# Kernel tuning notes

Hardware: AMD Instinct MI355X
Metric: run time of the kernel (lower is better)

The kernel has to match this reference:

```python
import jax, jax.numpy as jnp
import numpy as np

N = 100000      # nodes
E = 1600000     # edges (avg degree 16)
R = 4           # num_relations
NB = 30         # num_bases
F_IN = 86       # num_node_features
H = 128         # hidden_dim
C = 18          # N_CLASSES
G = 512         # graphs in batch


def setup_inputs() -> dict:
    key = jax.random.key(0)
    ks = jax.random.split(key, 14)
    x = jax.random.normal(ks[0], (N, F_IN), dtype=jnp.float32)
    edge_index = jax.random.randint(ks[1], (2, E), 0, N, dtype=jnp.int32)
    edge_type = jax.random.randint(ks[2], (E,), 0, R, dtype=jnp.int32)
    batch = jnp.sort(jax.random.randint(ks[3], (N,), 0, G, dtype=jnp.int32))
    s_in = 1.0 / np.sqrt(F_IN)
    s_h = 1.0 / np.sqrt(H)
    s_b = 1.0 / np.sqrt(NB)
    basis1 = jax.random.normal(ks[4], (NB, F_IN, H), jnp.float32) * s_in
    comp1 = jax.random.normal(ks[5], (R, NB), jnp.float32) * s_b
    root1 = jax.random.normal(ks[6], (F_IN, H), jnp.float32) * s_in
    bias1 = jnp.zeros((H,), jnp.float32)
    basis2 = jax.random.normal(ks[7], (NB, H, H), jnp.float32) * s_h
    comp2 = jax.random.normal(ks[8], (R, NB), jnp.float32) * s_b
    root2 = jax.random.normal(ks[9], (H, H), jnp.float32) * s_h
    bias2 = jnp.zeros((H,), jnp.float32)
    fc_w = jax.random.normal(ks[10], (H, C), jnp.float32) * s_h
    fc_b = jnp.zeros((C,), jnp.float32)
    return {"x": x, "edge_index": edge_index, "edge_type": edge_type, "batch": batch,
            "basis1": basis1, "comp1": comp1, "root1": root1, "bias1": bias1,
            "basis2": basis2, "comp2": comp2, "root2": root2, "bias2": bias2,
            "fc_w": fc_w, "fc_b": fc_b}


def rgcn_conv(x, edge_index, edge_type, basis, comp, root, bias):
    # PyG RGCNConv with basis decomposition, aggr='mean' (per-relation mean, summed over relations)
    n = x.shape[0]
    W = jnp.einsum('rb,bio->rio', comp, basis)          # [R, in, out]
    xw = jnp.einsum('ni,rio->rno', x, W)                # [R, N, out] relation-specific transforms
    src, dst = edge_index[0], edge_index[1]
    msg = xw[edge_type, src]                            # [E, out] gather per edge
    seg = edge_type.astype(jnp.int32) * n + dst          # segment per (relation, dst-node)
    sums = jax.ops.segment_sum(msg, seg, num_segments=R * n)          # [R*N, out]
    cnt = jax.ops.segment_sum(jnp.ones((msg.shape[0],), msg.dtype), seg, num_segments=R * n)
    mean = sums / jnp.maximum(cnt, 1.0)[:, None]
    agg = mean.reshape(R, n, -1).sum(axis=0)            # sum over relations
    return agg + x @ root + bias


def reference(x, edge_index, edge_type, batch, basis1, comp1, root1, bias1,
              basis2, comp2, root2, bias2, fc_w, fc_b):
    h = jax.nn.relu(rgcn_conv(x, edge_index, edge_type, basis1, comp1, root1, bias1))
    h = rgcn_conv(h, edge_index, edge_type, basis2, comp2, root2, bias2)
    g = jax.ops.segment_sum(h, batch, num_segments=G)   # global_add_pool -> [G, H]
    g = jax.nn.relu(g @ fc_w + fc_b)
    # dropout is identity in eval mode
    return jax.nn.log_softmax(g, axis=1)
```

## Files before the change

### kernel.cpp

```cpp
#include <hip/hip_runtime.h>
#include <hip/hip_bf16.h>
#include <cstddef>
#include <cstdint>

#define N_NODES 100000
#define N_ROWS  100032
#define DUMMY   100000
#define N_EDGES 1600000
#define N_REL   4
#define N_BASES 30
#define FIN     86
#define HID     128
#define N_CLS   18
#define N_GRAPH 512
#define KCAT    640
#define BM      32
#define NKK     (KCAT / 32)

#define SEG (N_REL * N_NODES)
#define SSRC_MAX (N_EDGES + 3 * SEG)
#define SCAN_CHUNK 1024
#define NB_SCAN ((SEG + SCAN_CHUNK - 1) / SCAN_CHUNK)

typedef __attribute__((ext_vector_type(8))) short bf16x8;
typedef __attribute__((ext_vector_type(4))) float f32x4;

__device__ inline float blo(unsigned int u) {
    union { unsigned int i; float f; } c; c.i = u << 16; return c.f;
}
__device__ inline float bhi(unsigned int u) {
    union { unsigned int i; float f; } c; c.i = u & 0xffff0000u; return c.f;
}
__device__ inline unsigned short f2bf(float f) {
    __hip_bfloat16 h = __float2bfloat16(f);
    return *reinterpret_cast<unsigned short*>(&h);
}
__device__ inline unsigned int pk2(float lo, float hi) {
    return (unsigned int)f2bf(lo) | ((unsigned int)f2bf(hi) << 16);
}
__device__ inline int pad4i(int x) { return (x + 3) & ~3; }

template <int KV>
__global__ void k_wt(const float* __restrict__ basis, const float* __restrict__ comp,
                     const float* __restrict__ root, short* __restrict__ Wt) {
    int id = blockIdx.x * 256 + threadIdx.x;
    if (id >= KCAT * HID) return;
    int n = id & 127, s = id >> 7;
    int k = s & 127, blk = s >> 7;
    float v = 0.f;
    if (k < KV) {
        if (blk < N_REL) {
#pragma unroll
            for (int b = 0; b < N_BASES; ++b)
                v += comp[blk * N_BASES + b] * basis[((size_t)b * KV + k) * HID + n];
        } else {
            v = root[k * HID + n];
        }
    }
    Wt[(size_t)n * KCAT + s] = (short)f2bf(v);
}

__global__ void k_xcvt(const float* __restrict__ x, short* __restrict__ X0,
                       short* __restrict__ H1) {
    int id = blockIdx.x * 256 + threadIdx.x;
    if (id >= N_ROWS * HID) return;
    int n = id >> 7, k = id & 127;
    float v = (n < N_NODES && k < FIN) ? x[n * FIN + k] : 0.f;
    X0[id] = (short)f2bf(v);
    if (n >= N_NODES) H1[id] = 0;
}

__global__ void k_fill(int* __restrict__ p) {
    int i = blockIdx.x * 256 + threadIdx.x;
    if (i < SSRC_MAX) p[i] = DUMMY;
}

__global__ void k_count(const int* __restrict__ et, const int* __restrict__ dst,
                        int* __restrict__ cnt, int* __restrict__ rank) {
    int e = blockIdx.x * 256 + threadIdx.x;
    if (e >= N_EDGES) return;
    rank[e] = atomicAdd(cnt + et[e] * N_NODES + dst[e], 1);
}

__global__ void k_bsum(const int* __restrict__ cnt, int* __restrict__ bsum) {
    __shared__ int red[256];
    int base = blockIdx.x * SCAN_CHUNK + threadIdx.x * 4;
    int s = 0;
#pragma unroll
    for (int j = 0; j < 4; j++) { int idx = base + j; if (idx < SEG) s += pad4i(cnt[idx]); }
    red[threadIdx.x] = s;
    __syncthreads();
    for (int w = 128; w > 0; w >>= 1) {
        if (threadIdx.x < w) red[threadIdx.x] += red[threadIdx.x + w];
        __syncthreads();
    }
    if (threadIdx.x == 0) bsum[blockIdx.x] = red[0];
}

__global__ void k_bpref(int* __restrict__ bsum, int nb) {
    __shared__ int s[512];
    int t = threadIdx.x;
    int v = (t < nb) ? bsum[t] : 0;
    s[t] = v;
    __syncthreads();
    for (int d = 1; d < 512; d <<= 1) {
        int add = (t >= d) ? s[t - d] : 0;
        __syncthreads();
        s[t] += add;
        __syncthreads();
    }
    if (t < nb) bsum[t] = s[t] - v;
}

__global__ void k_offsets(const int* __restrict__ cnt, const int* __restrict__ bpref,
                          int* __restrict__ off) {
    __shared__ int tp[256];
    int t = threadIdx.x;
    int base = blockIdx.x * SCAN_CHUNK + t * 4;
    int v[4], s = 0;
#pragma unroll
    for (int j = 0; j < 4; j++) { int idx = base + j; v[j] = (idx < SEG) ? pad4i(cnt[idx]) : 0; s += v[j]; }
    tp[t] = s;
    __syncthreads();
    if (t == 0) { int run = 0; for (int i = 0; i < 256; i++) { int x = tp[i]; tp[i] = run; run += x; } }
    __syncthreads();
    int p = bpref[blockIdx.x] + tp[t];
#pragma unroll
    for (int j = 0; j < 4; j++) { int idx = base + j; if (idx < SEG) off[idx] = p; p += v[j]; }
}

__global__ void k_scatter(const int* __restrict__ et, const int* __restrict__ srcI,
                          const int* __restrict__ dstI, const int* __restrict__ off,
                          const int* __restrict__ rank, int* __restrict__ ssrc) {
    int e = blockIdx.x * 256 + threadIdx.x;
    if (e >= N_EDGES) return;
    int seg = et[e] * N_NODES + dstI[e];
    ssrc[off[seg] + rank[e]] = srcI[e];
}

template <int MODE>
__launch_bounds__(512, 4)
__global__ void k_fused(const short* __restrict__ F,
                        const int* __restrict__ off, const int* __restrict__ cnt,
                        const int* __restrict__ ssrc,
                        const short* __restrict__ Wt,
                        const float* __restrict__ bias,
                        short* __restrict__ H,
                        const int* __restrict__ batch, float* __restrict__ g) {
    __shared__ short As[BM * KCAT];
    char* Ab = reinterpret_cast<char*>(As);
    const int tid = threadIdx.x;
    const int m0 = blockIdx.x * BM;

    {
        const int row = tid >> 4, cu = tid & 15;
        uint4 v = *reinterpret_cast<const uint4*>(F + (size_t)(m0 + row) * HID + cu * 8);
        const int p = (row * 1280 + 1024 + cu * 16) ^ ((row & 7) << 4);
        *reinterpret_cast<uint4*>(Ab + p) = v;
    }

    {
        const int G = tid >> 4, q = tid & 15;
        const int node = m0 + G;
        if (node < N_NODES) {
            const int pbase = G * 1280 + q * 16;
            const int swz = (G & 7) << 4;
            for (int r = 0; r < N_REL; ++r) {
                const int seg = r * N_NODES + node;
                const int o0 = off[seg], c = cnt[seg];
                float a[8];
#pragma unroll
                for (int j = 0; j < 8; ++j) a[j] = 0.f;
                const int4* sp = reinterpret_cast<const int4*>(ssrc + o0);
                const int nch = (c + 3) >> 2;
                for (int ch = 0; ch < nch; ++ch) {
                    int4 e4 = sp[ch];
                    uint4 v0 = *reinterpret_cast<const uint4*>(F + (size_t)e4.x * HID + q * 8);
                    uint4 v1 = *reinterpret_cast<const uint4*>(F + (size_t)e4.y * HID + q * 8);
                    uint4 v2 = *reinterpret_cast<const uint4*>(F + (size_t)e4.z * HID + q * 8);
                    uint4 v3 = *reinterpret_cast<const uint4*>(F + (size_t)e4.w * HID + q * 8);
                    a[0] += blo(v0.x) + blo(v1.x) + blo(v2.x) + blo(v3.x);
                    a[1] += bhi(v0.x) + bhi(v1.x) + bhi(v2.x) + bhi(v3.x);
                    a[2] += blo(v0.y) + blo(v1.y) + blo(v2.y) + blo(v3.y);
                    a[3] += bhi(v0.y) + bhi(v1.y) + bhi(v2.y) + bhi(v3.y);
                    a[4] += blo(v0.z) + blo(v1.z) + blo(v2.z) + blo(v3.z);
                    a[5] += bhi(v0.z) + bhi(v1.z) + bhi(v2.z) + bhi(v3.z);
                    a[6] += blo(v0.w) + blo(v1.w) + blo(v2.w) + blo(v3.w);
                    a[7] += bhi(v0.w) + bhi(v1.w) + bhi(v2.w) + bhi(v3.w);
                }
                const float inv = (c > 0) ? 1.f / (float)c : 0.f;
                uint4 w;
                w.x = pk2(a[0] * inv, a[1] * inv);
                w.y = pk2(a[2] * inv, a[3] * inv);
                w.z = pk2(a[4] * inv, a[5] * inv);
                w.w = pk2(a[6] * inv, a[7] * inv);
                *reinterpret_cast<uint4*>(Ab + ((pbase + r * 256) ^ swz)) = w;
            }
        }
    }
    __syncthreads();

    const int wave = tid >> 6, lane = tid & 63;
    const int q = lane & 15, hi = lane >> 4;
    const int col = wave * 16 + q;

    bf16x8 bfrag[NKK];
    {
        const short* bp = Wt + (size_t)col * KCAT + hi * 8;
#pragma unroll
        for (int kk = 0; kk < NKK; ++kk)
            bfrag[kk] = *reinterpret_cast<const bf16x8*>(bp + kk * 32);
    }

    f32x4 acc[2];
    acc[0] = (f32x4){0.f, 0.f, 0.f, 0.f};
    acc[1] = (f32x4){0.f, 0.f, 0.f, 0.f};
    const int arow = q * 1280;
    const int bx = (hi * 16) ^ ((q & 7) << 4);
#pragma unroll
    for (int kk = 0; kk < NKK; ++kk) {
        const int bo = (kk * 64) ^ bx;
#pragma unroll
        for (int rf = 0; rf < 2; ++rf) {
            bf16x8 a = *reinterpret_cast<const bf16x8*>(Ab + arow + rf * (16 * 1280) + bo);
            acc[rf] = __builtin_amdgcn_mfma_f32_16x16x32_bf16(a, bfrag[kk], acc[rf], 0, 0, 0);
        }
    }

    if (MODE == 1) {
        const float bc = bias[col];
#pragma unroll
        for (int rf = 0; rf < 2; ++rf) {
#pragma unroll
            for (int r = 0; r < 4; ++r) {
                const int row = m0 + rf * 16 + hi * 4 + r;
                if (row < N_NODES) {
                    float v = fmaxf(acc[rf][r] + bc, 0.f);
                    H[(size_t)row * HID + col] = (short)f2bf(v);
                }
            }
        }
    } else {
        int curb = -1;
        float run = 0.f;
#pragma unroll
        for (int rf = 0; rf < 2; ++rf) {
#pragma unroll
            for (int r = 0; r < 4; ++r) {
                const int row = m0 + rf * 16 + hi * 4 + r;
                if (row < N_NODES) {
                    int b = batch[row];
                    if (b != curb) {
                        if (curb >= 0) atomicAdd(&g[curb * HID + col], run);
                        curb = b; run = 0.f;
                    }
                    run += acc[rf][r];
                }
            }
        }
        if (curb >= 0) atomicAdd(&g[curb * HID + col], run);
    }
}

__global__ void k_fc(const float* __restrict__ g, const float* __restrict__ bias2,
                     const int* __restrict__ batch, const float* __restrict__ fcw,
                     const float* __restrict__ fcb, float* __restrict__ out) {
    __shared__ float pooled[HID];
    __shared__ float vals[N_CLS];
    __shared__ float s_lse;
    __shared__ int s_cnt;
    int gi = blockIdx.x, t = threadIdx.x;
    if (t == 0) {
        int lo = 0, hi = N_NODES;
        while (lo < hi) { int m = (lo + hi) >> 1; if (batch[m] < gi) lo = m + 1; else hi = m; }
        int lo2 = lo, hi2 = N_NODES;
        while (lo2 < hi2) { int m = (lo2 + hi2) >> 1; if (batch[m] < gi + 1) lo2 = m + 1; else hi2 = m; }
        s_cnt = lo2 - lo;
    }
    __syncthreads();
    pooled[t] = g[gi * HID + t] + (float)s_cnt * bias2[t];
    __syncthreads();
    if (t < N_CLS) {
        float acc = fcb[t];
        for (int k = 0; k < HID; k++) acc = fmaf(pooled[k], fcw[k * N_CLS + t], acc);
        vals[t] = fmaxf(acc, 0.f);
    }
    __syncthreads();
    if (t == 0) {
        float m = vals[0];
        for (int c = 1; c < N_CLS; c++) m = fmaxf(m, vals[c]);
        float ssum = 0.f;
        for (int c = 0; c < N_CLS; c++) ssum += expf(vals[c] - m);
        s_lse = m + logf(ssum);
    }
    __syncthreads();
    if (t < N_CLS) out[gi * N_CLS + t] = vals[t] - s_lse;
}

extern "C" void kernel_launch(void* const* d_in, const int* in_sizes, int n_in,
                              void* d_out, int out_size, void* d_ws, size_t ws_size,
                              hipStream_t stream) {
    const float* x      = (const float*)d_in[0];
    const int*   ei     = (const int*)d_in[1];
    const int*   src    = ei;
    const int*   dst    = ei + N_EDGES;
    const int*   et     = (const int*)d_in[2];
    const int*   batch  = (const int*)d_in[3];
    const float* basis1 = (const float*)d_in[4];
    const float* comp1  = (const float*)d_in[5];
    const float* root1  = (const float*)d_in[6];
    const float* bias1  = (const float*)d_in[7];
    const float* basis2 = (const float*)d_in[8];
    const float* comp2  = (const float*)d_in[9];
    const float* root2  = (const float*)d_in[10];
    const float* bias2  = (const float*)d_in[11];
    const float* fcw    = (const float*)d_in[12];
    const float* fcb    = (const float*)d_in[13];
    float* out = (float*)d_out;

    short* X0   = (short*)d_ws;
    short* H1   = X0 + (size_t)N_ROWS * HID;
    short* Wt1  = H1 + (size_t)N_ROWS * HID;
    short* Wt2  = Wt1 + HID * KCAT;
    float* g    = (float*)(Wt2 + HID * KCAT);
    int*   cnt  = (int*)(g + N_GRAPH * HID);
    int*   off  = cnt + SEG;
    int*   bsum = off + SEG;
    int*   rank = bsum + 512;
    int*   ssrc = rank + N_EDGES;

    hipMemsetAsync(cnt, 0, SEG * sizeof(int), stream);
    hipMemsetAsync(g, 0, (size_t)N_GRAPH * HID * sizeof(float), stream);

    k_wt<FIN><<<(KCAT * HID + 255) / 256, 256, 0, stream>>>(basis1, comp1, root1, Wt1);
    k_wt<HID><<<(KCAT * HID + 255) / 256, 256, 0, stream>>>(basis2, comp2, root2, Wt2);
    k_xcvt<<<(N_ROWS * HID + 255) / 256, 256, 0, stream>>>(x, X0, H1);
    k_fill<<<(SSRC_MAX + 255) / 256, 256, 0, stream>>>(ssrc);

    k_count<<<(N_EDGES + 255) / 256, 256, 0, stream>>>(et, dst, cnt, rank);
    k_bsum<<<NB_SCAN, 256, 0, stream>>>(cnt, bsum);
    k_bpref<<<1, 512, 0, stream>>>(bsum, NB_SCAN);
    k_offsets<<<NB_SCAN, 256, 0, stream>>>(cnt, bsum, off);
    k_scatter<<<(N_EDGES + 255) / 256, 256, 0, stream>>>(et, src, dst, off, rank, ssrc);

    const int FUSED_GRID = N_ROWS / BM;

    k_fused<1><<<FUSED_GRID, 512, 0, stream>>>(X0, off, cnt, ssrc, Wt1, bias1, H1,
                                               nullptr, nullptr);
    k_fused<2><<<FUSED_GRID, 512, 0, stream>>>(H1, off, cnt, ssrc, Wt2, nullptr, nullptr,
                                               batch, g);

    k_fc<<<N_GRAPH, HID, 0, stream>>>(g, bias2, batch, fcw, fcb, out);
}
```

Measured before the change: 391.3 us.

## Fuse prep kernels, interleave relation segments per node, aggregate two relations concurrently

Merges the memsets, weight-combination, input conversion and ssrc fill into a single prep kernel to cut launch count. Reorders the (relation,dst) segment index to dst*4+rel, so each node's four offsets and counts are read with one int4 load and its edge lists sit next to each other. The aggregation now walks two relations at once with dummy-padded indices, giving eight independent gathers in flight per step. In exchange, padded iterations do extra dummy-row loads when relation degrees differ, and the weight loop is no longer unrolled.

```diff
diff --git a/kernel.cpp b/kernel.cpp
--- a/kernel.cpp
+++ b/kernel.cpp
@@ -19,11 +19,13 @@
 
 #define SEG (N_REL * N_NODES)
 #define SSRC_MAX (N_EDGES + 3 * SEG)
+#define SSRC_ALLOC (SSRC_MAX + 64)
 #define SCAN_CHUNK 1024
 #define NB_SCAN ((SEG + SCAN_CHUNK - 1) / SCAN_CHUNK)
 
 typedef __attribute__((ext_vector_type(8))) short bf16x8;
 typedef __attribute__((ext_vector_type(4))) float f32x4;
+typedef __attribute__((ext_vector_type(2))) float f32x2;
 
 __device__ inline float blo(unsigned int u) {
     union { unsigned int i; float f; } c; c.i = u << 16; return c.f;
@@ -31,6 +33,7 @@
 __device__ inline float bhi(unsigned int u) {
     union { unsigned int i; float f; } c; c.i = u & 0xffff0000u; return c.f;
 }
+__device__ inline f32x2 ubf2(unsigned int u) { return (f32x2){blo(u), bhi(u)}; }
 __device__ inline unsigned short f2bf(float f) {
     __hip_bfloat16 h = __float2bfloat16(f);
     return *reinterpret_cast<unsigned short*>(&h);
@@ -40,17 +43,22 @@
 }
 __device__ inline int pad4i(int x) { return (x + 3) & ~3; }
 
-template <int KV>
-__global__ void k_wt(const float* __restrict__ basis, const float* __restrict__ comp,
-                     const float* __restrict__ root, short* __restrict__ Wt) {
-    int id = blockIdx.x * 256 + threadIdx.x;
-    if (id >= KCAT * HID) return;
+#define PREP_R0 (N_ROWS * HID)
+#define PREP_R1 (KCAT * HID)
+#define PREP_R2 (KCAT * HID)
+#define PREP_R3 SSRC_ALLOC
+#define PREP_R4 SEG
+#define PREP_R5 (N_GRAPH * HID)
+#define PREP_TOTAL (PREP_R0 + PREP_R1 + PREP_R2 + PREP_R3 + PREP_R4 + PREP_R5)
+
+__device__ inline void wt_body(int id, int KV, const float* __restrict__ basis,
+                               const float* __restrict__ comp, const float* __restrict__ root,
+                               short* __restrict__ Wt) {
     int n = id & 127, s = id >> 7;
     int k = s & 127, blk = s >> 7;
     float v = 0.f;
     if (k < KV) {
         if (blk < N_REL) {
-#pragma unroll
             for (int b = 0; b < N_BASES; ++b)
                 v += comp[blk * N_BASES + b] * basis[((size_t)b * KV + k) * HID + n];
         } else {
@@ -60,26 +68,40 @@
     Wt[(size_t)n * KCAT + s] = (short)f2bf(v);
 }
 
-__global__ void k_xcvt(const float* __restrict__ x, short* __restrict__ X0,
-                       short* __restrict__ H1) {
+__global__ void k_prep(const float* __restrict__ x,
+                       const float* __restrict__ basis1, const float* __restrict__ comp1,
+                       const float* __restrict__ root1,
+                       const float* __restrict__ basis2, const float* __restrict__ comp2,
+                       const float* __restrict__ root2,
+                       short* __restrict__ X0, short* __restrict__ H1,
+                       short* __restrict__ Wt1, short* __restrict__ Wt2,
+                       int* __restrict__ ssrc, int* __restrict__ cnt,
+                       float* __restrict__ g) {
     int id = blockIdx.x * 256 + threadIdx.x;
-    if (id >= N_ROWS * HID) return;
-    int n = id >> 7, k = id & 127;
-    float v = (n < N_NODES && k < FIN) ? x[n * FIN + k] : 0.f;
-    X0[id] = (short)f2bf(v);
-    if (n >= N_NODES) H1[id] = 0;
-}
-
-__global__ void k_fill(int* __restrict__ p) {
-    int i = blockIdx.x * 256 + threadIdx.x;
-    if (i < SSRC_MAX) p[i] = DUMMY;
+    if (id < PREP_R0) {
+        int n = id >> 7, k = id & 127;
+        float v = (n < N_NODES && k < FIN) ? x[n * FIN + k] : 0.f;
+        X0[id] = (short)f2bf(v);
+        if (n >= N_NODES) H1[id] = 0;
+        return;
+    }
+    id -= PREP_R0;
+    if (id < PREP_R1) { wt_body(id, FIN, basis1, comp1, root1, Wt1); return; }
+    id -= PREP_R1;
+    if (id < PREP_R2) { wt_body(id, HID, basis2, comp2, root2, Wt2); return; }
+    id -= PREP_R2;
+    if (id < PREP_R3) { ssrc[id] = DUMMY; return; }
+    id -= PREP_R3;
+    if (id < PREP_R4) { cnt[id] = 0; return; }
+    id -= PREP_R4;
+    if (id < PREP_R5) g[id] = 0.f;
 }
 
 __global__ void k_count(const int* __restrict__ et, const int* __restrict__ dst,
                         int* __restrict__ cnt, int* __restrict__ rank) {
     int e = blockIdx.x * 256 + threadIdx.x;
     if (e >= N_EDGES) return;
-    rank[e] = atomicAdd(cnt + et[e] * N_NODES + dst[e], 1);
+    rank[e] = atomicAdd(cnt + dst[e] * 4 + et[e], 1);
 }
 
 __global__ void k_bsum(const int* __restrict__ cnt, int* __restrict__ bsum) {
@@ -134,8 +156,56 @@
                           const int* __restrict__ rank, int* __restrict__ ssrc) {
     int e = blockIdx.x * 256 + threadIdx.x;
     if (e >= N_EDGES) return;
-    int seg = et[e] * N_NODES + dstI[e];
+    int seg = dstI[e] * 4 + et[e];
     ssrc[off[seg] + rank[e]] = srcI[e];
+}
+
+#define ACCROW(A, v) { A[0] += ubf2(v.x); A[1] += ubf2(v.y); A[2] += ubf2(v.z); A[3] += ubf2(v.w); }
+
+__device__ __forceinline__ void agg_pair(const short* __restrict__ F,
+                                         const int* __restrict__ ssrc,
+                                         int oa, int ca, int ob, int cb,
+                                         char* Ab, int G, int q, int ra) {
+    f32x2 A0[4], A1[4];
+#pragma unroll
+    for (int j = 0; j < 4; ++j) { A0[j] = (f32x2){0.f, 0.f}; A1[j] = (f32x2){0.f, 0.f}; }
+    const int na = (ca + 3) >> 2, nb = (cb + 3) >> 2;
+    const int ia = oa >> 2, ib = ob >> 2;
+    const int nmax = na > nb ? na : nb;
+    const int4* sp = reinterpret_cast<const int4*>(ssrc);
+    const int cq = q * 8;
+    for (int t = 0; t < nmax; ++t) {
+        int4 ea = sp[ia + (t < na ? t : 0)];
+        int4 eb = sp[ib + (t < nb ? t : 0)];
+        ea.x = t < na ? ea.x : DUMMY; ea.y = t < na ? ea.y : DUMMY;
+        ea.z = t < na ? ea.z : DUMMY; ea.w = t < na ? ea.w : DUMMY;
+        eb.x = t < nb ? eb.x : DUMMY; eb.y = t < nb ? eb.y : DUMMY;
+        eb.z = t < nb ? eb.z : DUMMY; eb.w = t < nb ? eb.w : DUMMY;
+        const uint4 va0 = *reinterpret_cast<const uint4*>(F + (size_t)ea.x * HID + cq);
+        const uint4 va1 = *reinterpret_cast<const uint4*>(F + (size_t)ea.y * HID + cq);
+        const uint4 va2 = *reinterpret_cast<const uint4*>(F + (size_t)ea.z * HID + cq);
+        const uint4 va3 = *reinterpret_cast<const uint4*>(F + (size_t)ea.w * HID + cq);
+        const uint4 vb0 = *reinterpret_cast<const uint4*>(F + (size_t)eb.x * HID + cq);
+        const uint4 vb1 = *reinterpret_cast<const uint4*>(F + (size_t)eb.y * HID + cq);
+        const uint4 vb2 = *reinterpret_cast<const uint4*>(F + (size_t)eb.z * HID + cq);
+        const uint4 vb3 = *reinterpret_cast<const uint4*>(F + (size_t)eb.w * HID + cq);
+        ACCROW(A0, va0); ACCROW(A0, va1); ACCROW(A0, va2); ACCROW(A0, va3);
+        ACCROW(A1, vb0); ACCROW(A1, vb1); ACCROW(A1, vb2); ACCROW(A1, vb3);
+    }
+    const float inva = (ca > 0) ? 1.f / (float)ca : 0.f;
+    const float invb = (cb > 0) ? 1.f / (float)cb : 0.f;
+    uint4 wa, wb;
+    wa.x = pk2(A0[0].x * inva, A0[0].y * inva);
+    wa.y = pk2(A0[1].x * inva, A0[1].y * inva);
+    wa.z = pk2(A0[2].x * inva, A0[2].y * inva);
+    wa.w = pk2(A0[3].x * inva, A0[3].y * inva);
+    wb.x = pk2(A1[0].x * invb, A1[0].y * invb);
+    wb.y = pk2(A1[1].x * invb, A1[1].y * invb);
+    wb.z = pk2(A1[2].x * invb, A1[2].y * invb);
+    wb.w = pk2(A1[3].x * invb, A1[3].y * invb);
+    const int swz = (G & 7) << 4;
+    *reinterpret_cast<uint4*>(Ab + (G * 1280 + ((ra * 256 + q * 16) ^ swz))) = wa;
+    *reinterpret_cast<uint4*>(Ab + (G * 1280 + (((ra + 1) * 256 + q * 16) ^ swz))) = wb;
 }
 
 template <int MODE>
@@ -163,39 +233,10 @@
         const int G = tid >> 4, q = tid & 15;
         const int node = m0 + G;
         if (node < N_NODES) {
-            const int pbase = G * 1280 + q * 16;
-            const int swz = (G & 7) << 4;
-            for (int r = 0; r < N_REL; ++r) {
-                const int seg = r * N_NODES + node;
-                const int o0 = off[seg], c = cnt[seg];
-                float a[8];
-#pragma unroll
-                for (int j = 0; j < 8; ++j) a[j] = 0.f;
-                const int4* sp = reinterpret_cast<const int4*>(ssrc + o0);
-                const int nch = (c + 3) >> 2;
-                for (int ch = 0; ch < nch; ++ch) {
-                    int4 e4 = sp[ch];
-                    uint4 v0 = *reinterpret_cast<const uint4*>(F + (size_t)e4.x * HID + q * 8);
-                    uint4 v1 = *reinterpret_cast<const uint4*>(F + (size_t)e4.y * HID + q * 8);
-                    uint4 v2 = *reinterpret_cast<const uint4*>(F + (size_t)e4.z * HID + q * 8);
-                    uint4 v3 = *reinterpret_cast<const uint4*>(F + (size_t)e4.w * HID + q * 8);
-                    a[0] += blo(v0.x) + blo(v1.x) + blo(v2.x) + blo(v3.x);
-                    a[1] += bhi(v0.x) + bhi(v1.x) + bhi(v2.x) + bhi(v3.x);
-                    a[2] += blo(v0.y) + blo(v1.y) + blo(v2.y) + blo(v3.y);
-                    a[3] += bhi(v0.y) + bhi(v1.y) + bhi(v2.y) + bhi(v3.y);
-                    a[4] += blo(v0.z) + blo(v1.z) + blo(v2.z) + blo(v3.z);
-                    a[5] += bhi(v0.z) + bhi(v1.z) + bhi(v2.z) + bhi(v3.z);
-                    a[6] += blo(v0.w) + blo(v1.w) + blo(v2.w) + blo(v3.w);
-                    a[7] += bhi(v0.w) + bhi(v1.w) + bhi(v2.w) + bhi(v3.w);
-                }
-                const float inv = (c > 0) ? 1.f / (float)c : 0.f;
-                uint4 w;
-                w.x = pk2(a[0] * inv, a[1] * inv);
-                w.y = pk2(a[2] * inv, a[3] * inv);
-                w.z = pk2(a[4] * inv, a[5] * inv);
-                w.w = pk2(a[6] * inv, a[7] * inv);
-                *reinterpret_cast<uint4*>(Ab + ((pbase + r * 256) ^ swz)) = w;
-            }
+            const int4 o4 = *reinterpret_cast<const int4*>(off + node * 4);
+            const int4 c4 = *reinterpret_cast<const int4*>(cnt + node * 4);
+            agg_pair(F, ssrc, o4.x, c4.x, o4.y, c4.y, Ab, G, q, 0);
+            agg_pair(F, ssrc, o4.z, c4.z, o4.w, c4.w, Ab, G, q, 2);
         }
     }
     __syncthreads();
@@ -329,13 +370,9 @@
     int*   rank = bsum + 512;
     int*   ssrc = rank + N_EDGES;
 
-    hipMemsetAsync(cnt, 0, SEG * sizeof(int), stream);
-    hipMemsetAsync(g, 0, (size_t)N_GRAPH * HID * sizeof(float), stream);
-
-    k_wt<FIN><<<(KCAT * HID + 255) / 256, 256, 0, stream>>>(basis1, comp1, root1, Wt1);
-    k_wt<HID><<<(KCAT * HID + 255) / 256, 256, 0, stream>>>(basis2, comp2, root2, Wt2);
-    k_xcvt<<<(N_ROWS * HID + 255) / 256, 256, 0, stream>>>(x, X0, H1);
-    k_fill<<<(SSRC_MAX + 255) / 256, 256, 0, stream>>>(ssrc);
+    k_prep<<<(PREP_TOTAL + 255) / 256, 256, 0, stream>>>(
+        x, basis1, comp1, root1, basis2, comp2, root2,
+        X0, H1, Wt1, Wt2, ssrc, cnt, g);
 
     k_count<<<(N_EDGES + 255) / 256, 256, 0, stream>>>(et, dst, cnt, rank);
     k_bsum<<<NB_SCAN, 256, 0, stream>>>(cnt, bsum);
```

Result: no change. 395.1 us (+1.0%).

## Build CSR via per-tile counting sort and merge prep kernels

Applied to the files above, without the earlier changes.

Replaces the global per-(relation,node) counting-sort CSR build, which needed atomics on a 400K-entry counter array, a multi-kernel scan and a full DUMMY fill, with a two-level scheme. Edges are first bucketed per 32-node tile with atomics on a small tile counter array and a single-block scan. Each tile is then sorted locally in shared memory by (node, relation), and the sort writes node-major off/cnt arrays plus its own padding. Weight building, feature conversion and zeroing are merged into one prep kernel. The fused kernels now load four offsets per node as an int4 and prefetch the first index chunks. The cost is an extra intermediate edge buffer pass, and the local sort serialises a 128-bucket prefix on one thread.

```diff
diff --git a/kernel.cpp b/kernel.cpp
--- a/kernel.cpp
+++ b/kernel.cpp
@@ -17,10 +17,11 @@
 #define BM      32
 #define NKK     (KCAT / 32)
 
-#define SEG (N_REL * N_NODES)
-#define SSRC_MAX (N_EDGES + 3 * SEG)
-#define SCAN_CHUNK 1024
-#define NB_SCAN ((SEG + SCAN_CHUNK - 1) / SCAN_CHUNK)
+#define NTILE   (N_ROWS / BM)
+#define NTILEP  3200
+#define TPAD    (3 * 128)
+#define SEGP    (NTILE * 128)
+#define SSRC_ALLOC (N_EDGES + NTILE * (TPAD + 4) + 64)
 
 typedef __attribute__((ext_vector_type(8))) short bf16x8;
 typedef __attribute__((ext_vector_type(4))) float f32x4;
@@ -38,19 +39,22 @@
 __device__ inline unsigned int pk2(float lo, float hi) {
     return (unsigned int)f2bf(lo) | ((unsigned int)f2bf(hi) << 16);
 }
-__device__ inline int pad4i(int x) { return (x + 3) & ~3; }
-
-template <int KV>
-__global__ void k_wt(const float* __restrict__ basis, const float* __restrict__ comp,
-                     const float* __restrict__ root, short* __restrict__ Wt) {
-    int id = blockIdx.x * 256 + threadIdx.x;
-    if (id >= KCAT * HID) return;
+
+#define PREP_R0 (N_ROWS * HID)
+#define PREP_R1 (KCAT * HID)
+#define PREP_R2 (KCAT * HID)
+#define PREP_R3 NTILEP
+#define PREP_R4 (N_GRAPH * HID)
+#define PREP_TOTAL (PREP_R0 + PREP_R1 + PREP_R2 + PREP_R3 + PREP_R4)
+
+__device__ inline void wt_body(int id, int KV, const float* __restrict__ basis,
+                               const float* __restrict__ comp, const float* __restrict__ root,
+                               short* __restrict__ Wt) {
     int n = id & 127, s = id >> 7;
     int k = s & 127, blk = s >> 7;
     float v = 0.f;
     if (k < KV) {
         if (blk < N_REL) {
-#pragma unroll
             for (int b = 0; b < N_BASES; ++b)
                 v += comp[blk * N_BASES + b] * basis[((size_t)b * KV + k) * HID + n];
         } else {
@@ -60,82 +64,149 @@
     Wt[(size_t)n * KCAT + s] = (short)f2bf(v);
 }
 
-__global__ void k_xcvt(const float* __restrict__ x, short* __restrict__ X0,
-                       short* __restrict__ H1) {
+__global__ void k_prep(const float* __restrict__ x,
+                       const float* __restrict__ basis1, const float* __restrict__ comp1,
+                       const float* __restrict__ root1,
+                       const float* __restrict__ basis2, const float* __restrict__ comp2,
+                       const float* __restrict__ root2,
+                       short* __restrict__ X0, short* __restrict__ H1,
+                       short* __restrict__ Wt1, short* __restrict__ Wt2,
+                       int* __restrict__ tilecnt, float* __restrict__ g) {
     int id = blockIdx.x * 256 + threadIdx.x;
-    if (id >= N_ROWS * HID) return;
-    int n = id >> 7, k = id & 127;
-    float v = (n < N_NODES && k < FIN) ? x[n * FIN + k] : 0.f;
-    X0[id] = (short)f2bf(v);
-    if (n >= N_NODES) H1[id] = 0;
-}
-
-__global__ void k_fill(int* __restrict__ p) {
-    int i = blockIdx.x * 256 + threadIdx.x;
-    if (i < SSRC_MAX) p[i] = DUMMY;
-}
-
-__global__ void k_count(const int* __restrict__ et, const int* __restrict__ dst,
-                        int* __restrict__ cnt, int* __restrict__ rank) {
+    if (id < PREP_R0) {
+        int n = id >> 7, k = id & 127;
+        float v = (n < N_NODES && k < FIN) ? x[n * FIN + k] : 0.f;
+        X0[id] = (short)f2bf(v);
+        if (n >= N_NODES) H1[id] = 0;
+        return;
+    }
+    id -= PREP_R0;
+    if (id < PREP_R1) { wt_body(id, FIN, basis1, comp1, root1, Wt1); return; }
+    id -= PREP_R1;
+    if (id < PREP_R2) { wt_body(id, HID, basis2, comp2, root2, Wt2); return; }
+    id -= PREP_R2;
+    if (id < PREP_R3) { tilecnt[id] = 0; return; }
+    id -= PREP_R3;
+    if (id < PREP_R4) g[id] = 0.f;
+}
+
+__global__ void k_tilecnt(const int* __restrict__ dst, int* __restrict__ tilecnt,
+                          int* __restrict__ rank) {
     int e = blockIdx.x * 256 + threadIdx.x;
     if (e >= N_EDGES) return;
-    rank[e] = atomicAdd(cnt + et[e] * N_NODES + dst[e], 1);
-}
-
-__global__ void k_bsum(const int* __restrict__ cnt, int* __restrict__ bsum) {
-    __shared__ int red[256];
-    int base = blockIdx.x * SCAN_CHUNK + threadIdx.x * 4;
-    int s = 0;
-#pragma unroll
-    for (int j = 0; j < 4; j++) { int idx = base + j; if (idx < SEG) s += pad4i(cnt[idx]); }
-    red[threadIdx.x] = s;
-    __syncthreads();
-    for (int w = 128; w > 0; w >>= 1) {
-        if (threadIdx.x < w) red[threadIdx.x] += red[threadIdx.x + w];
+    rank[e] = atomicAdd(tilecnt + (dst[e] >> 5), 1);
+}
+
+__global__ void k_tilescan(const int* __restrict__ tilecnt, int* __restrict__ rawoff,
+                           int* __restrict__ obase) {
+    __shared__ int s1[1024], s2[1024];
+    int t = threadIdx.x;
+    int base = t * 4;
+    int v[4], w[4], sum1 = 0, sum2 = 0;
+#pragma unroll
+    for (int j = 0; j < 4; ++j) {
+        v[j] = (base + j < NTILE) ? tilecnt[base + j] : 0;
+        w[j] = ((v[j] + 3) & ~3) + TPAD;
+        sum1 += v[j]; sum2 += w[j];
+    }
+    s1[t] = sum1; s2[t] = sum2;
+    __syncthreads();
+    for (int d = 1; d < 1024; d <<= 1) {
+        int a1 = (t >= d) ? s1[t - d] : 0;
+        int a2 = (t >= d) ? s2[t - d] : 0;
         __syncthreads();
-    }
-    if (threadIdx.x == 0) bsum[blockIdx.x] = red[0];
-}
-
-__global__ void k_bpref(int* __restrict__ bsum, int nb) {
-    __shared__ int s[512];
-    int t = threadIdx.x;
-    int v = (t < nb) ? bsum[t] : 0;
-    s[t] = v;
-    __syncthreads();
-    for (int d = 1; d < 512; d <<= 1) {
-        int add = (t >= d) ? s[t - d] : 0;
+        s1[t] += a1; s2[t] += a2;
         __syncthreads();
-        s[t] += add;
-        __syncthreads();
-    }
-    if (t < nb) bsum[t] = s[t] - v;
-}
-
-__global__ void k_offsets(const int* __restrict__ cnt, const int* __restrict__ bpref,
-                          int* __restrict__ off) {
-    __shared__ int tp[256];
-    int t = threadIdx.x;
-    int base = blockIdx.x * SCAN_CHUNK + t * 4;
-    int v[4], s = 0;
-#pragma unroll
-    for (int j = 0; j < 4; j++) { int idx = base + j; v[j] = (idx < SEG) ? pad4i(cnt[idx]) : 0; s += v[j]; }
-    tp[t] = s;
-    __syncthreads();
-    if (t == 0) { int run = 0; for (int i = 0; i < 256; i++) { int x = tp[i]; tp[i] = run; run += x; } }
-    __syncthreads();
-    int p = bpref[blockIdx.x] + tp[t];
-#pragma unroll
-    for (int j = 0; j < 4; j++) { int idx = base + j; if (idx < SEG) off[idx] = p; p += v[j]; }
-}
-
-__global__ void k_scatter(const int* __restrict__ et, const int* __restrict__ srcI,
-                          const int* __restrict__ dstI, const int* __restrict__ off,
-                          const int* __restrict__ rank, int* __restrict__ ssrc) {
+    }
+    int p1 = s1[t] - sum1, p2 = s2[t] - sum2;
+#pragma unroll
+    for (int j = 0; j < 4; ++j) {
+        if (base + j < NTILE) {
+            rawoff[base + j] = p1;
+            obase[base + j] = p2;
+            p1 += v[j]; p2 += w[j];
+        }
+    }
+}
+
+__global__ void k_tilescatter(const int* __restrict__ et, const int* __restrict__ srcI,
+                              const int* __restrict__ dstI, const int* __restrict__ rank,
+                              const int* __restrict__ rawoff, int2* __restrict__ ebuf) {
     int e = blockIdx.x * 256 + threadIdx.x;
     if (e >= N_EDGES) return;
-    int seg = et[e] * N_NODES + dstI[e];
-    ssrc[off[seg] + rank[e]] = srcI[e];
+    int d = dstI[e];
+    int t = d >> 5;
+    int key = ((d & 31) << 2) | et[e];
+    int2 rec; rec.x = srcI[e]; rec.y = key;
+    ebuf[rawoff[t] + rank[e]] = rec;
+}
+
+__global__ void k_tilesort(const int2* __restrict__ ebuf, const int* __restrict__ tilecnt,
+                           const int* __restrict__ rawoff, const int* __restrict__ obase,
+                           int* __restrict__ ssrc, int* __restrict__ off,
+                           int* __restrict__ cnt) {
+    __shared__ int hist[128], boff[128], cur[128];
+    const int t = blockIdx.x, tid = threadIdx.x;
+    const int n = tilecnt[t];
+    const int base_in = rawoff[t];
+    const int base_out = obase[t];
+    if (tid < 128) { hist[tid] = 0; cur[tid] = 0; }
+    __syncthreads();
+    for (int i = tid; i < n; i += 256)
+        atomicAdd(&hist[ebuf[base_in + i].y], 1);
+    __syncthreads();
+    if (tid == 0) {
+        int run = 0;
+        for (int b = 0; b < 128; ++b) { boff[b] = run; run += (hist[b] + 3) & ~3; }
+    }
+    __syncthreads();
+    for (int i = tid; i < n; i += 256) {
+        int2 e = ebuf[base_in + i];
+        int p = atomicAdd(&cur[e.y], 1);
+        ssrc[base_out + boff[e.y] + p] = e.x;
+    }
+    if (tid < 128) {
+        int b = tid, h = hist[b], bo = base_out + boff[b];
+        int hp = (h + 3) & ~3;
+        for (int j = h; j < hp; ++j) ssrc[bo + j] = DUMMY;
+        off[t * 128 + b] = bo;
+        cnt[t * 128 + b] = h;
+    }
+}
+
+__device__ __forceinline__ void agg_one(const short* __restrict__ F,
+                                        const int4* __restrict__ sp,
+                                        int o, int c, int4 e4,
+                                        char* Ab, int G, int q, int r) {
+    float a[8];
+#pragma unroll
+    for (int j = 0; j < 8; ++j) a[j] = 0.f;
+    const int cq = q * 8;
+    const int nch = (c + 3) >> 2;
+    const int ib = o >> 2;
+    for (int ch = 0; ch < nch; ++ch) {
+        if (ch) e4 = sp[ib + ch];
+        uint4 v0 = *reinterpret_cast<const uint4*>(F + (size_t)e4.x * HID + cq);
+        uint4 v1 = *reinterpret_cast<const uint4*>(F + (size_t)e4.y * HID + cq);
+        uint4 v2 = *reinterpret_cast<const uint4*>(F + (size_t)e4.z * HID + cq);
+        uint4 v3 = *reinterpret_cast<const uint4*>(F + (size_t)e4.w * HID + cq);
+        a[0] += blo(v0.x); a[1] += bhi(v0.x); a[2] += blo(v0.y); a[3] += bhi(v0.y);
+        a[4] += blo(v0.z); a[5] += bhi(v0.z); a[6] += blo(v0.w); a[7] += bhi(v0.w);
+        a[0] += blo(v1.x); a[1] += bhi(v1.x); a[2] += blo(v1.y); a[3] += bhi(v1.y);
+        a[4] += blo(v1.z); a[5] += bhi(v1.z); a[6] += blo(v1.w); a[7] += bhi(v1.w);
+        a[0] += blo(v2.x); a[1] += bhi(v2.x); a[2] += blo(v2.y); a[3] += bhi(v2.y);
+        a[4] += blo(v2.z); a[5] += bhi(v2.z); a[6] += blo(v2.w); a[7] += bhi(v2.w);
+        a[0] += blo(v3.x); a[1] += bhi(v3.x); a[2] += blo(v3.y); a[3] += bhi(v3.y);
+        a[4] += blo(v3.z); a[5] += bhi(v3.z); a[6] += blo(v3.w); a[7] += bhi(v3.w);
+    }
+    const float inv = (c > 0) ? 1.f / (float)c : 0.f;
+    uint4 w;
+    w.x = pk2(a[0] * inv, a[1] * inv);
+    w.y = pk2(a[2] * inv, a[3] * inv);
+    w.z = pk2(a[4] * inv, a[5] * inv);
+    w.w = pk2(a[6] * inv, a[7] * inv);
+    const int swz = (G & 7) << 4;
+    *reinterpret_cast<uint4*>(Ab + (G * 1280 + ((r * 256 + q * 16) ^ swz))) = w;
 }
 
 template <int MODE>
@@ -151,58 +222,35 @@
     char* Ab = reinterpret_cast<char*>(As);
     const int tid = threadIdx.x;
     const int m0 = blockIdx.x * BM;
+    const int G = tid >> 4, q = tid & 15;
+    const int node = m0 + G;
+
+    int4 o4 = (int4){0, 0, 0, 0}, c4 = (int4){0, 0, 0, 0};
+    const int4* sp = reinterpret_cast<const int4*>(ssrc);
+    if (node < N_NODES) {
+        o4 = *reinterpret_cast<const int4*>(off + node * 4);
+        c4 = *reinterpret_cast<const int4*>(cnt + node * 4);
+    }
+    int4 pre0 = sp[o4.x >> 2];
+    int4 pre1 = sp[o4.y >> 2];
 
     {
-        const int row = tid >> 4, cu = tid & 15;
-        uint4 v = *reinterpret_cast<const uint4*>(F + (size_t)(m0 + row) * HID + cu * 8);
-        const int p = (row * 1280 + 1024 + cu * 16) ^ ((row & 7) << 4);
+        uint4 v = *reinterpret_cast<const uint4*>(F + (size_t)(m0 + G) * HID + q * 8);
+        const int p = (G * 1280 + 1024 + q * 16) ^ ((G & 7) << 4);
         *reinterpret_cast<uint4*>(Ab + p) = v;
     }
 
-    {
-        const int G = tid >> 4, q = tid & 15;
-        const int node = m0 + G;
-        if (node < N_NODES) {
-            const int pbase = G * 1280 + q * 16;
-            const int swz = (G & 7) << 4;
-            for (int r = 0; r < N_REL; ++r) {
-                const int seg = r * N_NODES + node;
-                const int o0 = off[seg], c = cnt[seg];
-                float a[8];
-#pragma unroll
-                for (int j = 0; j < 8; ++j) a[j] = 0.f;
-                const int4* sp = reinterpret_cast<const int4*>(ssrc + o0);
-                const int nch = (c + 3) >> 2;
-                for (int ch = 0; ch < nch; ++ch) {
-                    int4 e4 = sp[ch];
-                    uint4 v0 = *reinterpret_cast<const uint4*>(F + (size_t)e4.x * HID + q * 8);
-                    uint4 v1 = *reinterpret_cast<const uint4*>(F + (size_t)e4.y * HID + q * 8);
-                    uint4 v2 = *reinterpret_cast<const uint4*>(F + (size_t)e4.z * HID + q * 8);
-                    uint4 v3 = *reinterpret_cast<const uint4*>(F + (size_t)e4.w * HID + q * 8);
-                    a[0] += blo(v0.x) + blo(v1.x) + blo(v2.x) + blo(v3.x);
-                    a[1] += bhi(v0.x) + bhi(v1.x) + bhi(v2.x) + bhi(v3.x);
-                    a[2] += blo(v0.y) + blo(v1.y) + blo(v2.y) + blo(v3.y);
-                    a[3] += bhi(v0.y) + bhi(v1.y) + bhi(v2.y) + bhi(v3.y);
-                    a[4] += blo(v0.z) + blo(v1.z) + blo(v2.z) + blo(v3.z);
-                    a[5] += bhi(v0.z) + bhi(v1.z) + bhi(v2.z) + bhi(v3.z);
-                    a[6] += blo(v0.w) + blo(v1.w) + blo(v2.w) + blo(v3.w);
-                    a[7] += bhi(v0.w) + bhi(v1.w) + bhi(v2.w) + bhi(v3.w);
-                }
-                const float inv = (c > 0) ? 1.f / (float)c : 0.f;
-                uint4 w;
-                w.x = pk2(a[0] * inv, a[1] * inv);
-                w.y = pk2(a[2] * inv, a[3] * inv);
-                w.z = pk2(a[4] * inv, a[5] * inv);
-                w.w = pk2(a[6] * inv, a[7] * inv);
-                *reinterpret_cast<uint4*>(Ab + ((pbase + r * 256) ^ swz)) = w;
-            }
-        }
+    if (node < N_NODES) {
+        agg_one(F, sp, o4.x, c4.x, pre0, Ab, G, q, 0);
+        agg_one(F, sp, o4.y, c4.y, pre1, Ab, G, q, 1);
+        agg_one(F, sp, o4.z, c4.z, sp[o4.z >> 2], Ab, G, q, 2);
+        agg_one(F, sp, o4.w, c4.w, sp[o4.w >> 2], Ab, G, q, 3);
     }
     __syncthreads();
 
     const int wave = tid >> 6, lane = tid & 63;
-    const int q = lane & 15, hi = lane >> 4;
-    const int col = wave * 16 + q;
+    const int ql = lane & 15, hi = lane >> 4;
+    const int col = wave * 16 + ql;
 
     bf16x8 bfrag[NKK];
     {
@@ -215,8 +263,8 @@
     f32x4 acc[2];
     acc[0] = (f32x4){0.f, 0.f, 0.f, 0.f};
     acc[1] = (f32x4){0.f, 0.f, 0.f, 0.f};
-    const int arow = q * 1280;
-    const int bx = (hi * 16) ^ ((q & 7) << 4);
+    const int arow = ql * 1280;
+    const int bx = (hi * 16) ^ ((ql & 7) << 4);
 #pragma unroll
     for (int kk = 0; kk < NKK; ++kk) {
         const int bo = (kk * 64) ^ bx;
@@ -318,37 +366,33 @@
     const float* fcb    = (const float*)d_in[13];
     float* out = (float*)d_out;
 
-    short* X0   = (short*)d_ws;
-    short* H1   = X0 + (size_t)N_ROWS * HID;
-    short* Wt1  = H1 + (size_t)N_ROWS * HID;
-    short* Wt2  = Wt1 + HID * KCAT;
-    float* g    = (float*)(Wt2 + HID * KCAT);
-    int*   cnt  = (int*)(g + N_GRAPH * HID);
-    int*   off  = cnt + SEG;
-    int*   bsum = off + SEG;
-    int*   rank = bsum + 512;
-    int*   ssrc = rank + N_EDGES;
-
-    hipMemsetAsync(cnt, 0, SEG * sizeof(int), stream);
-    hipMemsetAsync(g, 0, (size_t)N_GRAPH * HID * sizeof(float), stream);
-
-    k_wt<FIN><<<(KCAT * HID + 255) / 256, 256, 0, stream>>>(basis1, comp1, root1, Wt1);
-    k_wt<HID><<<(KCAT * HID + 255) / 256, 256, 0, stream>>>(basis2, comp2, root2, Wt2);
-    k_xcvt<<<(N_ROWS * HID + 255) / 256, 256, 0, stream>>>(x, X0, H1);
-    k_fill<<<(SSRC_MAX + 255) / 256, 256, 0, stream>>>(ssrc);
-
-    k_count<<<(N_EDGES + 255) / 256, 256, 0, stream>>>(et, dst, cnt, rank);
-    k_bsum<<<NB_SCAN, 256, 0, stream>>>(cnt, bsum);
-    k_bpref<<<1, 512, 0, stream>>>(bsum, NB_SCAN);
-    k_offsets<<<NB_SCAN, 256, 0, stream>>>(cnt, bsum, off);
-    k_scatter<<<(N_EDGES + 255) / 256, 256, 0, stream>>>(et, src, dst, off, rank, ssrc);
-
-    const int FUSED_GRID = N_ROWS / BM;
-
-    k_fused<1><<<FUSED_GRID, 512, 0, stream>>>(X0, off, cnt, ssrc, Wt1, bias1, H1,
-                                               nullptr, nullptr);
-    k_fused<2><<<FUSED_GRID, 512, 0, stream>>>(H1, off, cnt, ssrc, Wt2, nullptr, nullptr,
-                                               batch, g);
+    short* X0      = (short*)d_ws;
+    short* H1      = X0 + (size_t)N_ROWS * HID;
+    short* Wt1     = H1 + (size_t)N_ROWS * HID;
+    short* Wt2     = Wt1 + HID * KCAT;
+    float* g       = (float*)(Wt2 + HID * KCAT);
+    int*   cnt     = (int*)(g + N_GRAPH * HID);
+    int*   off     = cnt + SEGP;
+    int*   tilecnt = off + SEGP;
+    int*   rawoff  = tilecnt + NTILEP;
+    int*   obase   = rawoff + NTILEP;
+    int*   rank    = obase + NTILEP;
+    int2*  ebuf    = (int2*)(rank + N_EDGES);
+    int*   ssrc    = (int*)(ebuf + N_EDGES);
+
+    k_prep<<<(PREP_TOTAL + 255) / 256, 256, 0, stream>>>(
+        x, basis1, comp1, root1, basis2, comp2, root2,
+        X0, H1, Wt1, Wt2, tilecnt, g);
+
+    k_tilecnt<<<(N_EDGES + 255) / 256, 256, 0, stream>>>(dst, tilecnt, rank);
+    k_tilescan<<<1, 1024, 0, stream>>>(tilecnt, rawoff, obase);
+    k_tilescatter<<<(N_EDGES + 255) / 256, 256, 0, stream>>>(et, src, dst, rank, rawoff, ebuf);
+    k_tilesort<<<NTILE, 256, 0, stream>>>(ebuf, tilecnt, rawoff, obase, ssrc, off, cnt);
+
+    k_fused<1><<<NTILE, 512, 0, stream>>>(X0, off, cnt, ssrc, Wt1, bias1, H1,
+                                          nullptr, nullptr);
+    k_fused<2><<<NTILE, 512, 0, stream>>>(H1, off, cnt, ssrc, Wt2, nullptr, nullptr,
+                                          batch, g);
 
     k_fc<<<N_GRAPH, HID, 0, stream>>>(g, bias2, batch, fcw, fcb, out);
 }
```

Result: slower. 452.0 us (+15.5%).
